# Optimization experiments

Hardware: AMD Instinct MI355X
Metric: run time of the kernel (lower is better)

The kernel has to match this reference:

```python
import jax, jax.numpy as jnp
import numpy as np

B, H, W, C = 4, 64, 64, 512
LN_EPS = 1e-3  # keras LayerNormalization default epsilon


def setup_inputs() -> dict:
    key = jax.random.key(0)
    ks = jax.random.split(key, 10)
    s = 1.0 / np.sqrt(C)
    return {
        "x": jax.random.normal(ks[0], (B, H, W, C), dtype=jnp.float32),
        "ln_g": jnp.ones((C,), jnp.float32),
        "ln_b": jnp.zeros((C,), jnp.float32),
        "Wq": jax.random.normal(ks[1], (C, C), jnp.float32) * s,
        "bq": jnp.zeros((C,), jnp.float32),
        "Wk": jax.random.normal(ks[2], (C, C), jnp.float32) * s,
        "bk": jnp.zeros((C,), jnp.float32),
        "Wv": jax.random.normal(ks[3], (C, C), jnp.float32) * s,
        "bv": jnp.zeros((C,), jnp.float32),
        "Wp": jax.random.normal(ks[4], (C, C), jnp.float32) * s,
        "bp": jnp.zeros((C,), jnp.float32),
    }


def reference(x, ln_g, ln_b, Wq, bq, Wk, bk, Wv, bv, Wp, bp):
    b, h_, w_, c = x.shape
    n = h_ * w_
    # LayerNorm over channel axis (keras default axis=-1, eps=1e-3)
    mu = jnp.mean(x, axis=-1, keepdims=True)
    var = jnp.var(x, axis=-1, keepdims=True)
    hn = (x - mu) * jax.lax.rsqrt(var + LN_EPS) * ln_g + ln_b
    hf = hn.reshape(b, n, c)
    q = hf @ Wq + bq  # [b, n, c]
    k = hf @ Wk + bk
    v = hf @ Wv + bv
    scale = 1.0 / jnp.sqrt(jnp.asarray(c, x.dtype))
    scores = jnp.einsum("bqc,bkc->bqk", q, k) * scale  # [b, n, n]
    attn = jax.nn.softmax(scores, axis=-1)
    o = jnp.einsum("bqk,bkc->bqc", attn, v)  # [b, n, c]
    o = o @ Wp + bp
    return x + o.reshape(b, h_, w_, c)
```

## Files before the change

### kernel.cpp

```cpp
#include <hip/hip_runtime.h>
#include <cstdint>
#include <cmath>

typedef unsigned short u16;
typedef __attribute__((ext_vector_type(8))) short short8;
typedef __attribute__((ext_vector_type(4))) float f32x4;

#define BB 4
#define NTOK 4096
#define CDIM 512
#define NROWS (BB * NTOK)
#define QSCALE 0.0441941738241592f

__device__ __forceinline__ u16 f2bf(float f) {
  union { float f; uint32_t u; } v; v.f = f;
  return (u16)((v.u + 0x7fffu + ((v.u >> 16) & 1u)) >> 16);
}

__device__ __forceinline__ float bf2f(u16 u) {
  union { uint32_t u; float f; } v; v.u = (uint32_t)u << 16;
  return v.f;
}

__device__ __forceinline__ f32x4 mfma16(short8 a, short8 b, f32x4 c) {
  return __builtin_amdgcn_mfma_f32_16x16x32_bf16(a, b, c, 0, 0, 0);
}

__device__ __forceinline__ void gload16(const u16* g, u16* l) {
  __builtin_amdgcn_global_load_lds(
      (const __attribute__((address_space(1))) void*)g,
      (__attribute__((address_space(3))) void*)l, 16, 0, 0);
}

__global__ __launch_bounds__(256) void ln_kernel(const float* __restrict__ x,
                                                 const float* __restrict__ gam,
                                                 const float* __restrict__ bet,
                                                 u16* __restrict__ hn) {
  int row = blockIdx.x * 4 + (threadIdx.x >> 6);
  int lane = threadIdx.x & 63;
  const float4* xr = (const float4*)(x + (size_t)row * CDIM);
  float4 a0 = xr[lane];
  float4 a1 = xr[lane + 64];
  float s = a0.x + a0.y + a0.z + a0.w + a1.x + a1.y + a1.z + a1.w;
  float ss = a0.x * a0.x + a0.y * a0.y + a0.z * a0.z + a0.w * a0.w +
             a1.x * a1.x + a1.y * a1.y + a1.z * a1.z + a1.w * a1.w;
#pragma unroll
  for (int j = 0; j < 6; ++j) {
    s += __shfl_xor(s, 1 << j);
    ss += __shfl_xor(ss, 1 << j);
  }
  float mu = s * (1.0f / CDIM);
  float var = ss * (1.0f / CDIM) - mu * mu;
  float rs = rsqrtf(var + 1e-3f);
  const float4* g4 = (const float4*)gam;
  const float4* b4 = (const float4*)bet;
  float4 g0 = g4[lane], g1 = g4[lane + 64];
  float4 c0 = b4[lane], c1 = b4[lane + 64];
  u16* out = hn + (size_t)row * CDIM;
  ushort4 o0, o1;
  o0.x = f2bf((a0.x - mu) * rs * g0.x + c0.x);
  o0.y = f2bf((a0.y - mu) * rs * g0.y + c0.y);
  o0.z = f2bf((a0.z - mu) * rs * g0.z + c0.z);
  o0.w = f2bf((a0.w - mu) * rs * g0.w + c0.w);
  o1.x = f2bf((a1.x - mu) * rs * g1.x + c1.x);
  o1.y = f2bf((a1.y - mu) * rs * g1.y + c1.y);
  o1.z = f2bf((a1.z - mu) * rs * g1.z + c1.z);
  o1.w = f2bf((a1.w - mu) * rs * g1.w + c1.w);
  *(ushort4*)(out + lane * 4) = o0;
  *(ushort4*)(out + 256 + lane * 4) = o1;
}

__global__ __launch_bounds__(256) void wconv_kernel(
    const float* __restrict__ w0, const float* __restrict__ w1,
    const float* __restrict__ w2, const float* __restrict__ w3,
    const float* __restrict__ bq, const float* __restrict__ bk,
    const float* __restrict__ bv,
    u16* __restrict__ wt, float* __restrict__ bqkv) {
  __shared__ __align__(16) u16 tile[64][65];
  int which = blockIdx.z;
  const float* W = (which == 0) ? w0 : (which == 1) ? w1 : (which == 2) ? w2 : w3;
  float wscale = (which == 0) ? QSCALE : 1.0f;
  u16* WT = wt + (size_t)which * CDIM * CDIM;
  int kb = blockIdx.x * 64, nb = blockIdx.y * 64;
  int t = threadIdx.x;
  if (kb == 0 && which < 3 && t < 64) {
    const float* bs = (which == 0) ? bq : (which == 1) ? bk : bv;
    bqkv[which * CDIM + nb + t] = bs[nb + t] * wscale;
  }
#pragma unroll
  for (int i = 0; i < 16; ++i) {
    int idx = t + i * 256;
    int r = idx >> 6, c = idx & 63;
    tile[r][c] = f2bf(W[(size_t)(kb + r) * CDIM + nb + c] * wscale);
  }
  __syncthreads();
#pragma unroll
  for (int i = 0; i < 16; ++i) {
    int idx = t + i * 256;
    int r = idx >> 6, c = idx & 63;
    WT[(size_t)(nb + r) * CDIM + kb + c] = tile[c][r];
  }
}

__global__ __launch_bounds__(256) void vtrans_kernel(const u16* __restrict__ v,
                                                     int ld,
                                                     u16* __restrict__ vt) {
  __shared__ __align__(16) u16 tile[64][65];
  int nb = blockIdx.x * 64;
  int cb = blockIdx.y * 64;
  int b = blockIdx.z;
  int t = threadIdx.x;
  const u16* src = v + ((size_t)b * NTOK + nb) * ld + cb;
#pragma unroll
  for (int i = 0; i < 16; ++i) {
    int idx = t + i * 256;
    int r = idx >> 6, c = idx & 63;
    tile[r][c] = src[(size_t)r * ld + c];
  }
  __syncthreads();
  u16* dst = vt + ((size_t)b * CDIM + cb) * NTOK + nb;
#pragma unroll
  for (int i = 0; i < 16; ++i) {
    int idx = t + i * 256;
    int r = idx >> 6, c = idx & 63;
    dst[(size_t)r * NTOK + c] = tile[c][r];
  }
}

template <int MODE, int LOGSPLIT>
__global__ __launch_bounds__(512) void gemm256_kernel(
    const u16* __restrict__ A, int lda, size_t az,
    const u16* __restrict__ Bt, int ldb, size_t bz,
    const float* __restrict__ bias,
    const float* __restrict__ lsum, int lz,
    u16* __restrict__ outp, int ldo, size_t oz, size_t koz,
    int K) {
  __shared__ __align__(16) u16 lds[8][8192];
  int t = threadIdx.x;
  int w = t >> 6, lane = t & 63;
  int lr = lane & 15, lg = lane >> 4;
  int wr = w >> 2, wc = w & 3;
  int gx = gridDim.x, gy = gridDim.y;
  int nwg = gx * gy * (int)gridDim.z;
  int nlin = blockIdx.x + gx * (blockIdx.y + gy * blockIdx.z);
  int cpx = nwg >> 3;
  int swz = (nlin & 7) * cpx + (nlin >> 3);
  int bx = swz % gx;
  int rem = swz / gx;
  int by = rem % gy;
  int bz2 = rem / gy;
  int batch = bz2 >> LOGSPLIT;
  int kq = bz2 & ((1 << LOGSPLIT) - 1);
  size_t aoff = az * (size_t)batch + (size_t)kq * K;
  size_t boff = bz * (size_t)batch + (size_t)kq * K;
  size_t ooff = oz * (size_t)batch + koz * (size_t)kq;
  int lsrow0 = lz * batch;
  int mbase = by * 256, nbase = bx * 256;
  const f32x4 fz = {0.f, 0.f, 0.f, 0.f};
  f32x4 acc[8][4];
#pragma unroll
  for (int m = 0; m < 8; ++m)
#pragma unroll
    for (int n2 = 0; n2 < 4; ++n2) acc[m][n2] = fz;

  int srow = t >> 3;
  int scol = ((t & 7) ^ (srow & 7)) * 8;
  const u16* ga = A + aoff + (size_t)(mbase + srow) * lda + scol;
  const u16* gb = Bt + boff + (size_t)(nbase + srow) * ldb + scol;
  int pse0 = (lg ^ (lr & 7)) * 8;
  int pse1 = pse0 ^ 32;

#define STG_A(h, tile, d)                                              \
  {                                                                    \
    const u16* s_ = ga + (size_t)((h)*128) * lda + (tile)*64;          \
    u16* d_ = &lds[(d)*4 + (h)][0] + w * 512;                          \
    gload16(s_, d_);                                                   \
    gload16(s_ + (size_t)64 * lda, d_ + 4096);                        \
  }
#define STG_B(h, tile, d)                                              \
  {                                                                    \
    const u16* s_ = gb + (size_t)((h)*128) * ldb + (tile)*64;          \
    u16* d_ = &lds[(d)*4 + 2 + (h)][0] + w * 512;                      \
    gload16(s_, d_);                                                   \
    gload16(s_ + (size_t)64 * ldb, d_ + 4096);                        \
  }

#define RD_A(dst, d, mh)                                               \
  {                                                                    \
    const u16* p_ = &lds[(d)*4 + wr][0] + (((mh)*64 + lr) << 6);       \
    _Pragma("unroll") for (int m = 0; m < 4; ++m) {                    \
      dst[m * 2 + 0] = *(const short8*)(p_ + (m << 10) + pse0);        \
      dst[m * 2 + 1] = *(const short8*)(p_ + (m << 10) + pse1);        \
    }                                                                  \
  }
#define RD_B(dst, d, nh)                                               \
  {                                                                    \
    const u16* p_ = &lds[(d)*4 + 2 + (wc >> 1)][0] +                   \
                    (((wc & 1) * 64 + (nh)*32 + lr) << 6);             \
    _Pragma("unroll") for (int n2 = 0; n2 < 2; ++n2) {                 \
      dst[n2 * 2 + 0] = *(const short8*)(p_ + (n2 << 10) + pse0);      \
      dst[n2 * 2 + 1] = *(const short8*)(p_ + (n2 << 10) + pse1);      \
    }                                                                  \
  }

#define PHEND                                                          \
  asm volatile("" ::: "memory");                                       \
  __builtin_amdgcn_sched_barrier(0);                                   \
  __builtin_amdgcn_s_barrier();                                        \
  asm volatile("s_waitcnt lgkmcnt(0)" ::: "memory");                   \
  __builtin_amdgcn_sched_barrier(0);

#define VM2 asm volatile("s_waitcnt vmcnt(2)" ::: "memory");
#define VM0 asm volatile("s_waitcnt vmcnt(0)" ::: "memory");

#define MM(X, Y, mq, nq)                                               \
  __builtin_amdgcn_s_setprio(1);                                       \
  _Pragma("unroll") for (int m = 0; m < 4; ++m)                        \
      _Pragma("unroll") for (int n2 = 0; n2 < 2; ++n2)                 \
          _Pragma("unroll") for (int ks = 0; ks < 2; ++ks)             \
              acc[(mq)*4 + m][(nq)*2 + n2] =                           \
                  mfma16(X[m * 2 + ks], Y[n2 * 2 + ks],                \
                         acc[(mq)*4 + m][(nq)*2 + n2]);                \
  __builtin_amdgcn_s_setprio(0);

  short8 Af[8], Ag[8], Bf[4], Bg[4];
  int niter = K >> 7;

  STG_A(0, 0, 0); STG_A(1, 0, 0); STG_B(0, 0, 0); STG_B(1, 0, 0);
  STG_B(0, 1, 1);
  VM2;
  __builtin_amdgcn_s_barrier();
  asm volatile("" ::: "memory");
  __builtin_amdgcn_sched_barrier(0);

  for (int j = 0; j < niter; ++j) {
    int T1i = 2 * j + 1, T2i = 2 * j + 2, T3i = 2 * j + 3;
    bool more = (j + 1 < niter);
    RD_A(Af, 0, 0); RD_B(Bf, 0, 0);
    STG_B(1, T1i, 1);
    PHEND; MM(Af, Bf, 0, 0);
    RD_B(Bg, 0, 1);
    STG_A(0, T1i, 1);
    PHEND; MM(Af, Bg, 0, 1);
    RD_A(Ag, 0, 1);
    STG_A(1, T1i, 1);
    PHEND; MM(Ag, Bg, 1, 1);
    if (more) { STG_B(0, T2i, 0); VM2; } else { VM0; }
    PHEND; MM(Ag, Bf, 1, 0);
    RD_A(Af, 1, 0); RD_B(Bf, 1, 0);
    if (more) STG_B(1, T2i, 0);
    PHEND; MM(Af, Bf, 0, 0);
    RD_B(Bg, 1, 1);
    if (more) STG_A(0, T2i, 0);
    PHEND; MM(Af, Bg, 0, 1);
    RD_A(Ag, 1, 1);
    if (more) STG_A(1, T2i, 0);
    PHEND; MM(Ag, Bg, 1, 1);
    if (more) { STG_B(0, T3i, 1); VM2; } else { VM0; }
    PHEND; MM(Ag, Bf, 1, 0);
  }
#undef MM
#undef VM2
#undef VM0
#undef PHEND
#undef RD_A
#undef RD_B
#undef STG_A
#undef STG_B

  u16* op = outp + ooff;
#pragma unroll
  for (int m = 0; m < 8; ++m) {
    int grow = mbase + wr * 128 + m * 16 + lg * 4;
    float rl[4];
    if (MODE == 3) {
#pragma unroll
      for (int r = 0; r < 4; ++r)
        rl[r] = 1.0f / lsum[lsrow0 + grow + r];
    }
#pragma unroll
    for (int n2 = 0; n2 < 4; ++n2) {
      int gcol = nbase + wc * 64 + n2 * 16 + lr;
      float bnc = (MODE == 0) ? bias[gcol] : 0.f;
#pragma unroll
      for (int r = 0; r < 4; ++r) {
        size_t idx = (size_t)(grow + r) * ldo + gcol;
        float val = acc[m][n2][r];
        if (MODE == 0) {
          op[idx] = f2bf(val + bnc);
        } else if (MODE == 2) {
          op[idx] = f2bf(val);
        } else {
          op[idx] = f2bf(val * rl[r]);
        }
      }
    }
  }
}

__global__ __launch_bounds__(256) void gemm_fin_kernel(
    const u16* __restrict__ A, int lda,
    const u16* __restrict__ Bt, int ldb,
    const float* __restrict__ bias, const float* __restrict__ res,
    float* __restrict__ outp, int ldo, int K) {
  __shared__ __align__(16) u16 Als[2][128 * 32];
  __shared__ __align__(16) u16 Bls[2][128 * 32];
  int t = threadIdx.x;
  int w = t >> 6, lane = t & 63;
  int lr = lane & 15, lg = lane >> 4;
  int wr = w >> 1, wc = w & 1;
  int mbase = blockIdx.y * 128, nbase = blockIdx.x * 128;
  const f32x4 fz = {0.f, 0.f, 0.f, 0.f};
  f32x4 acc[4][4];
#pragma unroll
  for (int m = 0; m < 4; ++m)
#pragma unroll
    for (int n = 0; n < 4; ++n) acc[m][n] = fz;

  int scol = (((t & 3) ^ ((t >> 2) & 3) ^ ((t >> 4) & 1)) * 8);
  const u16* ga0 = A + (size_t)(mbase + (t >> 2)) * lda + scol;
  const u16* gb0 = Bt + (size_t)(nbase + (t >> 2)) * ldb + scol;
  int rsA = (lg ^ (lr & 3) ^ ((lr >> 2) & 1)) * 8;

#define STAGE(buf, ko)                                                 \
  {                                                                    \
    gload16(ga0 + (ko), &Als[buf][w * 512]);                           \
    gload16(ga0 + (size_t)64 * lda + (ko), &Als[buf][w * 512 + 2048]); \
    gload16(gb0 + (ko), &Bls[buf][w * 512]);                           \
    gload16(gb0 + (size_t)64 * ldb + (ko), &Bls[buf][w * 512 + 2048]); \
  }

  int nk = K >> 5;
  STAGE(0, 0);
  STAGE(1, 32);
  int cur = 0;
  for (int kt = 0; kt < nk; ++kt) {
    if (kt + 1 < nk) {
      asm volatile("s_waitcnt vmcnt(4)" ::: "memory");
    } else {
      asm volatile("s_waitcnt vmcnt(0)" ::: "memory");
    }
    __builtin_amdgcn_s_barrier();
    asm volatile("" ::: "memory");
    __builtin_amdgcn_sched_barrier(0);
    short8 af[4], bfr[4];
#pragma unroll
    for (int m = 0; m < 4; ++m)
      af[m] = *(const short8*)(&Als[cur][(wr * 64 + m * 16 + lr) * 32 + rsA]);
#pragma unroll
    for (int n = 0; n < 4; ++n)
      bfr[n] = *(const short8*)(&Bls[cur][(wc * 64 + n * 16 + lr) * 32 + rsA]);
#pragma unroll
    for (int m = 0; m < 4; ++m)
#pragma unroll
      for (int n = 0; n < 4; ++n)
        acc[m][n] = mfma16(af[m], bfr[n], acc[m][n]);
    asm volatile("s_waitcnt lgkmcnt(0)" ::: "memory");
    __builtin_amdgcn_s_barrier();
    asm volatile("" ::: "memory");
    if (kt + 2 < nk) STAGE(cur, (kt + 2) * 32);
    cur ^= 1;
  }
#undef STAGE

#pragma unroll
  for (int m = 0; m < 4; ++m) {
    int grow = mbase + wr * 64 + m * 16 + lg * 4;
#pragma unroll
    for (int n = 0; n < 4; ++n) {
      int gcol = nbase + wc * 64 + n * 16 + lr;
      float bnc = bias[gcol];
#pragma unroll
      for (int r = 0; r < 4; ++r) {
        size_t idx = (size_t)(grow + r) * ldo + gcol;
        outp[idx] = acc[m][n][r] + bnc + res[idx];
      }
    }
  }
}

__global__ __launch_bounds__(256) void softmax_kernel(u16* __restrict__ S,
                                                      float* __restrict__ lsum) {
  int row = blockIdx.x * 4 + (threadIdx.x >> 6);
  int lane = threadIdx.x & 63;
  u16* Sr = S + (size_t)row * NTOK;
  short8 d[8];
#pragma unroll
  for (int i = 0; i < 8; ++i)
    d[i] = *(const short8*)(Sr + i * 512 + lane * 8);
  float mx = -1e30f;
#pragma unroll
  for (int i = 0; i < 8; ++i)
#pragma unroll
    for (int j = 0; j < 8; ++j) mx = fmaxf(mx, bf2f((u16)d[i][j]));
#pragma unroll
  for (int j = 0; j < 6; ++j) mx = fmaxf(mx, __shfl_xor(mx, 1 << j));
  float sum = 0.f;
#pragma unroll
  for (int i = 0; i < 8; ++i) {
    short8 o;
#pragma unroll
    for (int j = 0; j < 8; ++j) {
      float p = __expf(bf2f((u16)d[i][j]) - mx);
      sum += p;
      o[j] = (short)f2bf(p);
    }
    *(short8*)(Sr + i * 512 + lane * 8) = o;
  }
#pragma unroll
  for (int j = 0; j < 6; ++j) sum += __shfl_xor(sum, 1 << j);
  if (lane == 0) lsum[row] = sum;
}

__global__ __launch_bounds__(256) void addp4_kernel(const u16* __restrict__ p,
                                                    size_t ss,
                                                    u16* __restrict__ ob) {
  size_t i = ((size_t)blockIdx.x * 256 + threadIdx.x) * 8;
  short8 a0 = *(const short8*)(p + i);
  short8 a1 = *(const short8*)(p + ss + i);
  short8 a2 = *(const short8*)(p + 2 * ss + i);
  short8 a3 = *(const short8*)(p + 3 * ss + i);
  short8 o;
#pragma unroll
  for (int j = 0; j < 8; ++j)
    o[j] = (short)f2bf(bf2f((u16)a0[j]) + bf2f((u16)a1[j]) +
                       bf2f((u16)a2[j]) + bf2f((u16)a3[j]));
  *(short8*)(ob + i) = o;
}

extern "C" void kernel_launch(void* const* d_in, const int* in_sizes, int n_in,
                              void* d_out, int out_size, void* d_ws, size_t ws_size,
                              hipStream_t stream) {
  (void)in_sizes; (void)n_in; (void)out_size;
  const float* x    = (const float*)d_in[0];
  const float* ln_g = (const float*)d_in[1];
  const float* ln_b = (const float*)d_in[2];
  const float* Wq   = (const float*)d_in[3];
  const float* bq   = (const float*)d_in[4];
  const float* Wk   = (const float*)d_in[5];
  const float* bk   = (const float*)d_in[6];
  const float* Wv   = (const float*)d_in[7];
  const float* bv   = (const float*)d_in[8];
  const float* Wp   = (const float*)d_in[9];
  const float* bp   = (const float*)d_in[10];

  const size_t MB = 1024ull * 1024ull;
  const size_t KB = 1024ull;
  char* ws = (char*)d_ws;
  u16* wt     = (u16*)(ws);
  float* bqkv = (float*)(ws + 2 * MB);
  float* ls   = (float*)(ws + 2 * MB + 64 * KB);
  u16* hn     = (u16*)(ws + 4 * MB);
  u16* qkv    = (u16*)(ws + 20 * MB);
  u16* vt     = (u16*)(ws + 68 * MB);
  bool full = ws_size >= 212 * MB;
  u16* S    = (u16*)(ws + 84 * MB);
  u16* part = (u16*)(ws + 4 * MB);
  u16* ob   = full ? vt : (u16*)(ws + 116 * MB);

  const float* nullf = nullptr;

  hipLaunchKernelGGL(wconv_kernel, dim3(8, 8, 4), dim3(256), 0, stream,
                     Wq, Wk, Wv, Wp, bq, bk, bv, wt, bqkv);
  hipLaunchKernelGGL(ln_kernel, dim3(NROWS / 4), dim3(256), 0, stream,
                     x, ln_g, ln_b, hn);
  hipLaunchKernelGGL((gemm256_kernel<0, 0>), dim3(6, 64, 1), dim3(512), 0,
                     stream, hn, CDIM, (size_t)0, wt, CDIM, (size_t)0,
                     bqkv, nullf, 0, qkv, 3 * CDIM, (size_t)0, (size_t)0, CDIM);
  hipLaunchKernelGGL(vtrans_kernel, dim3(64, 8, 4), dim3(256), 0, stream,
                     qkv + 2 * CDIM, 3 * CDIM, vt);

  if (full) {
    hipLaunchKernelGGL((gemm256_kernel<2, 0>), dim3(16, 16, 4), dim3(512), 0,
                       stream, qkv, 3 * CDIM, (size_t)NTOK * 3 * CDIM,
                       qkv + CDIM, 3 * CDIM, (size_t)NTOK * 3 * CDIM,
                       nullf, nullf, 0,
                       S, NTOK, (size_t)NTOK * NTOK, (size_t)0, CDIM);
    hipLaunchKernelGGL(softmax_kernel, dim3(4 * NTOK / 4), dim3(256), 0, stream,
                       S, ls);
    hipLaunchKernelGGL((gemm256_kernel<3, 2>), dim3(2, 16, 16), dim3(512), 0,
                       stream, S, NTOK, (size_t)NTOK * NTOK,
                       vt, NTOK, (size_t)CDIM * NTOK,
                       nullf, ls, NTOK,
                       part, CDIM, (size_t)NTOK * CDIM,
                       (size_t)NROWS * CDIM, NTOK / 4);
    hipLaunchKernelGGL(addp4_kernel, dim3(NROWS * CDIM / 2048), dim3(256), 0,
                       stream, part, (size_t)NROWS * CDIM, ob);
  } else {
    for (int p = 0; p < 4; ++p) {
      const u16* qp  = qkv + (size_t)p * NTOK * 3 * CDIM;
      const u16* kp  = qp + CDIM;
      const u16* vtp = vt + (size_t)p * CDIM * NTOK;
      u16* obp = ob + (size_t)p * NTOK * CDIM;
      float* lp = ls + (size_t)p * NTOK;
      hipLaunchKernelGGL((gemm256_kernel<2, 0>), dim3(16, 16, 1), dim3(512), 0,
                         stream, qp, 3 * CDIM, (size_t)0, kp, 3 * CDIM,
                         (size_t)0, nullf, nullf, 0,
                         S, NTOK, (size_t)0, (size_t)0, CDIM);
      hipLaunchKernelGGL(softmax_kernel, dim3(NTOK / 4), dim3(256), 0, stream,
                         S, lp);
      hipLaunchKernelGGL((gemm256_kernel<3, 0>), dim3(2, 16, 1), dim3(512), 0,
                         stream, S, NTOK, (size_t)0, vtp, NTOK, (size_t)0,
                         nullf, lp, 0,
                         obp, CDIM, (size_t)0, (size_t)0, NTOK);
    }
  }
  hipLaunchKernelGGL(gemm_fin_kernel, dim3(4, 128), dim3(256), 0, stream,
                     ob, CDIM, wt + 3 * CDIM * CDIM, CDIM,
                     bp, x, (float*)d_out, CDIM, CDIM);
}
```

Before: 292.3 us.

## Restructure GEMM pipeline with deeper prefetch and extra barrier per phase

```diff
diff --git a/kernel.cpp b/kernel.cpp
--- a/kernel.cpp
+++ b/kernel.cpp
@@ -203,14 +203,21 @@
     }                                                                  \
   }
 
-#define PHEND                                                          \
+#define PH_MID                                                         \
   asm volatile("" ::: "memory");                                       \
   __builtin_amdgcn_sched_barrier(0);                                   \
   __builtin_amdgcn_s_barrier();                                        \
   asm volatile("s_waitcnt lgkmcnt(0)" ::: "memory");                   \
   __builtin_amdgcn_sched_barrier(0);
 
-#define VM2 asm volatile("s_waitcnt vmcnt(2)" ::: "memory");
+#define PH_END                                                         \
+  asm volatile("" ::: "memory");                                       \
+  __builtin_amdgcn_sched_barrier(0);                                   \
+  __builtin_amdgcn_s_barrier();                                        \
+  asm volatile("" ::: "memory");                                       \
+  __builtin_amdgcn_sched_barrier(0);
+
+#define VM4 asm volatile("s_waitcnt vmcnt(4)" ::: "memory");
 #define VM0 asm volatile("s_waitcnt vmcnt(0)" ::: "memory");
 
 #define MM(X, Y, mq, nq)                                               \
@@ -227,42 +234,43 @@
   int niter = K >> 7;
 
   STG_A(0, 0, 0); STG_A(1, 0, 0); STG_B(0, 0, 0); STG_B(1, 0, 0);
-  STG_B(0, 1, 1);
-  VM2;
+  STG_B(0, 1, 1); STG_B(1, 1, 1);
+  VM4;
   __builtin_amdgcn_s_barrier();
   asm volatile("" ::: "memory");
   __builtin_amdgcn_sched_barrier(0);
 
   for (int j = 0; j < niter; ++j) {
-    int T1i = 2 * j + 1, T2i = 2 * j + 2, T3i = 2 * j + 3;
+    int t1 = 2 * j + 1, t2 = 2 * j + 2, t3 = 2 * j + 3;
     bool more = (j + 1 < niter);
     RD_A(Af, 0, 0); RD_B(Bf, 0, 0);
-    STG_B(1, T1i, 1);
-    PHEND; MM(Af, Bf, 0, 0);
+    STG_A(0, t1, 1);
+    PH_MID; MM(Af, Bf, 0, 0); PH_END;
     RD_B(Bg, 0, 1);
-    STG_A(0, T1i, 1);
-    PHEND; MM(Af, Bg, 0, 1);
+    STG_A(1, t1, 1);
+    PH_MID; MM(Af, Bg, 0, 1); PH_END;
     RD_A(Ag, 0, 1);
-    STG_A(1, T1i, 1);
-    PHEND; MM(Ag, Bg, 1, 1);
-    if (more) { STG_B(0, T2i, 0); VM2; } else { VM0; }
-    PHEND; MM(Ag, Bf, 1, 0);
+    if (more) STG_B(0, t2, 0);
+    PH_MID; MM(Ag, Bg, 1, 1); PH_END;
+    if (more) { STG_B(1, t2, 0); VM4; } else { VM0; }
+    PH_MID; MM(Ag, Bf, 1, 0); PH_END;
     RD_A(Af, 1, 0); RD_B(Bf, 1, 0);
-    if (more) STG_B(1, T2i, 0);
-    PHEND; MM(Af, Bf, 0, 0);
+    if (more) STG_A(0, t2, 0);
+    PH_MID; MM(Af, Bf, 0, 0); PH_END;
     RD_B(Bg, 1, 1);
-    if (more) STG_A(0, T2i, 0);
-    PHEND; MM(Af, Bg, 0, 1);
+    if (more) STG_A(1, t2, 0);
+    PH_MID; MM(Af, Bg, 0, 1); PH_END;
     RD_A(Ag, 1, 1);
-    if (more) STG_A(1, T2i, 0);
-    PHEND; MM(Ag, Bg, 1, 1);
-    if (more) { STG_B(0, T3i, 1); VM2; } else { VM0; }
-    PHEND; MM(Ag, Bf, 1, 0);
+    if (more) STG_B(0, t3, 1);
+    PH_MID; MM(Ag, Bg, 1, 1); PH_END;
+    if (more) { STG_B(1, t3, 1); VM4; } else { VM0; }
+    PH_MID; MM(Ag, Bf, 1, 0); PH_END;
   }
 #undef MM
-#undef VM2
+#undef VM4
 #undef VM0
-#undef PHEND
+#undef PH_MID
+#undef PH_END
 #undef RD_A
 #undef RD_B
 #undef STG_A
```

Measured after the change: 298.9 us. 1.02x slower.

## Restructure GEMM main loop prefetch schedule and halve split-K for PV

Applied to the files above, without the earlier changes.

```diff
diff --git a/kernel.cpp b/kernel.cpp
--- a/kernel.cpp
+++ b/kernel.cpp
@@ -203,15 +203,15 @@
     }                                                                  \
   }
 
-#define PHEND                                                          \
+#define BARX                                                           \
   asm volatile("" ::: "memory");                                       \
   __builtin_amdgcn_sched_barrier(0);                                   \
   __builtin_amdgcn_s_barrier();                                        \
-  asm volatile("s_waitcnt lgkmcnt(0)" ::: "memory");                   \
+  asm volatile("" ::: "memory");                                       \
   __builtin_amdgcn_sched_barrier(0);
 
+#define VM0 asm volatile("s_waitcnt vmcnt(0)" ::: "memory");
 #define VM2 asm volatile("s_waitcnt vmcnt(2)" ::: "memory");
-#define VM0 asm volatile("s_waitcnt vmcnt(0)" ::: "memory");
 
 #define MM(X, Y, mq, nq)                                               \
   __builtin_amdgcn_s_setprio(1);                                       \
@@ -227,42 +227,43 @@
   int niter = K >> 7;
 
   STG_A(0, 0, 0); STG_A(1, 0, 0); STG_B(0, 0, 0); STG_B(1, 0, 0);
-  STG_B(0, 1, 1);
+  STG_A(0, 1, 1);
   VM2;
   __builtin_amdgcn_s_barrier();
   asm volatile("" ::: "memory");
   __builtin_amdgcn_sched_barrier(0);
+  RD_A(Af, 0, 0); RD_B(Bf, 0, 0);
 
   for (int j = 0; j < niter; ++j) {
-    int T1i = 2 * j + 1, T2i = 2 * j + 2, T3i = 2 * j + 3;
+    int t1 = 2 * j + 1, t2 = 2 * j + 2, t3 = 2 * j + 3;
     bool more = (j + 1 < niter);
-    RD_A(Af, 0, 0); RD_B(Bf, 0, 0);
-    STG_B(1, T1i, 1);
-    PHEND; MM(Af, Bf, 0, 0);
-    RD_B(Bg, 0, 1);
-    STG_A(0, T1i, 1);
-    PHEND; MM(Af, Bg, 0, 1);
-    RD_A(Ag, 0, 1);
-    STG_A(1, T1i, 1);
-    PHEND; MM(Ag, Bg, 1, 1);
-    if (more) { STG_B(0, T2i, 0); VM2; } else { VM0; }
-    PHEND; MM(Ag, Bf, 1, 0);
+    RD_A(Ag, 0, 1); RD_B(Bg, 0, 1);
+    STG_A(1, t1, 1);
+    BARX; MM(Af, Bf, 0, 0);
+    STG_B(0, t1, 1); STG_B(1, t1, 1);
+    BARX; MM(Af, Bg, 0, 1);
+    VM0;
+    BARX; MM(Ag, Bf, 1, 0);
     RD_A(Af, 1, 0); RD_B(Bf, 1, 0);
-    if (more) STG_B(1, T2i, 0);
-    PHEND; MM(Af, Bf, 0, 0);
-    RD_B(Bg, 1, 1);
-    if (more) STG_A(0, T2i, 0);
-    PHEND; MM(Af, Bg, 0, 1);
-    RD_A(Ag, 1, 1);
-    if (more) STG_A(1, T2i, 0);
-    PHEND; MM(Ag, Bg, 1, 1);
-    if (more) { STG_B(0, T3i, 1); VM2; } else { VM0; }
-    PHEND; MM(Ag, Bf, 1, 0);
+    if (more) STG_A(0, t2, 0);
+    BARX; MM(Ag, Bg, 1, 1);
+    RD_A(Ag, 1, 1); RD_B(Bg, 1, 1);
+    if (more) STG_A(1, t2, 0);
+    BARX; MM(Af, Bf, 0, 0);
+    if (more) { STG_B(0, t2, 0); STG_B(1, t2, 0); }
+    BARX; MM(Af, Bg, 0, 1);
+    VM0;
+    BARX; MM(Ag, Bf, 1, 0);
+    if (more) {
+      RD_A(Af, 0, 0); RD_B(Bf, 0, 0);
+      STG_A(0, t3, 1);
+    }
+    BARX; MM(Ag, Bg, 1, 1);
   }
 #undef MM
+#undef VM0
 #undef VM2
-#undef VM0
-#undef PHEND
+#undef BARX
 #undef RD_A
 #undef RD_B
 #undef STG_A
@@ -412,19 +413,16 @@
   if (lane == 0) lsum[row] = sum;
 }
 
-__global__ __launch_bounds__(256) void addp4_kernel(const u16* __restrict__ p,
+__global__ __launch_bounds__(256) void addp2_kernel(const u16* __restrict__ p,
                                                     size_t ss,
                                                     u16* __restrict__ ob) {
   size_t i = ((size_t)blockIdx.x * 256 + threadIdx.x) * 8;
   short8 a0 = *(const short8*)(p + i);
   short8 a1 = *(const short8*)(p + ss + i);
-  short8 a2 = *(const short8*)(p + 2 * ss + i);
-  short8 a3 = *(const short8*)(p + 3 * ss + i);
   short8 o;
 #pragma unroll
   for (int j = 0; j < 8; ++j)
-    o[j] = (short)f2bf(bf2f((u16)a0[j]) + bf2f((u16)a1[j]) +
-                       bf2f((u16)a2[j]) + bf2f((u16)a3[j]));
+    o[j] = (short)f2bf(bf2f((u16)a0[j]) + bf2f((u16)a1[j]));
   *(short8*)(ob + i) = o;
 }
 
@@ -478,13 +476,13 @@
                        S, NTOK, (size_t)NTOK * NTOK, (size_t)0, CDIM);
     hipLaunchKernelGGL(softmax_kernel, dim3(4 * NTOK / 4), dim3(256), 0, stream,
                        S, ls);
-    hipLaunchKernelGGL((gemm256_kernel<3, 2>), dim3(2, 16, 16), dim3(512), 0,
+    hipLaunchKernelGGL((gemm256_kernel<3, 1>), dim3(2, 16, 8), dim3(512), 0,
                        stream, S, NTOK, (size_t)NTOK * NTOK,
                        vt, NTOK, (size_t)CDIM * NTOK,
                        nullf, ls, NTOK,
                        part, CDIM, (size_t)NTOK * CDIM,
-                       (size_t)NROWS * CDIM, NTOK / 4);
-    hipLaunchKernelGGL(addp4_kernel, dim3(NROWS * CDIM / 2048), dim3(256), 0,
+                       (size_t)NROWS * CDIM, NTOK / 2);
+    hipLaunchKernelGGL(addp2_kernel, dim3(NROWS * CDIM / 2048), dim3(256), 0,
                        stream, part, (size_t)NROWS * CDIM, ob);
   } else {
     for (int p = 0; p < 4; ++p) {
```

New measurement: 476.8 us. 1.63x slower.
